# Kernel optimization log

Measured on AMD Instinct MI355X. Metric: run time of the kernel, lower is better.

The kernel has to match this reference:

```python
import jax, jax.numpy as jnp
import numpy as np

N = 100000
E = 1600000
D_IN = 256
N_HEADS = 4
OUT_SZ = 32  # output_dim // n_heads = 128 // 4
ALPHA = 0.2  # leaky relu slope


def setup_inputs() -> dict:
    key = jax.random.key(0)
    ks = jax.random.split(key, 8)
    x = jax.random.normal(ks[0], (N, D_IN), dtype=jnp.float32)
    edge_row = jax.random.randint(ks[1], (E,), 0, N, dtype=jnp.int32)
    edge_col = jax.random.randint(ks[2], (E,), 0, N, dtype=jnp.int32)
    # per-head params: W (conv1d k=1, no bias), a1/a2 (conv1d k=1 with bias)
    W = jax.random.normal(ks[3], (N_HEADS, D_IN, OUT_SZ), dtype=jnp.float32) * (1.0 / np.sqrt(D_IN))
    a1 = jax.random.normal(ks[4], (N_HEADS, OUT_SZ), dtype=jnp.float32) * (1.0 / np.sqrt(OUT_SZ))
    b1 = jnp.zeros((N_HEADS,), dtype=jnp.float32)
    a2 = jax.random.normal(ks[5], (N_HEADS, OUT_SZ), dtype=jnp.float32) * (1.0 / np.sqrt(OUT_SZ))
    b2 = jnp.zeros((N_HEADS,), dtype=jnp.float32)
    return {"x": x, "W": W, "a1": a1, "b1": b1, "a2": a2, "b2": b2,
            "edge_row": edge_row, "edge_col": edge_col}


def _gat_heads(x, W, a1, b1, a2, b2, edge_row, edge_col):
    # per-head linear transform: [H, N, O]
    fts = jnp.einsum('nd,hdo->hno', x, W)
    f1 = jnp.einsum('hno,ho->hn', fts, a1) + b1[:, None]  # [H, N]
    f2 = jnp.einsum('hno,ho->hn', fts, a2) + b2[:, None]  # [H, N]
    # edge logits: f1[row] + f2[col]  (adj values are 1)
    logits = f1[:, edge_row] + f2[:, edge_col]            # [H, E]
    lr = jnp.maximum(ALPHA * logits, logits)
    # segment softmax over each node's incoming edge set (rows)
    seg_max = jax.vmap(lambda v: jax.ops.segment_max(v, edge_row, num_segments=N))(lr)
    ex = jnp.exp(lr - seg_max[:, edge_row])
    denom = jax.vmap(lambda v: jax.ops.segment_sum(v, edge_row, num_segments=N))(ex)
    coef = ex / denom[:, edge_row]                        # [H, E]
    # SpMM aggregation: out[h, i] = sum_{e: row(e)=i} coef[h,e] * fts[h, col(e)]
    msg = coef[:, :, None] * fts[:, edge_col, :]          # [H, E, O]
    agg = jax.vmap(lambda m: jax.ops.segment_sum(m, edge_row, num_segments=N))(msg)  # [H, N, O]
    h = jnp.transpose(agg, (1, 0, 2)).reshape(N, N_HEADS * OUT_SZ)  # concat heads
    return jax.nn.elu(h)[None]  # [1, N, output_dim]


def reference(x, W, a1, b1, a2, b2, edge_row, edge_col):
    return _gat_heads(x, W, a1, b1, a2, b2, edge_row, edge_col)
```

## Files before the change

### kernel.cpp

```cpp
#include <hip/hip_runtime.h>
#include <hip/hip_bf16.h>
#include <math.h>

#define ALPHA 0.2f
#define PB_EDGES 4096

typedef __attribute__((ext_vector_type(8))) short short8;
typedef __attribute__((ext_vector_type(4))) float floatx4;

__device__ __forceinline__ ushort f2bf(float f) {
    uint u = __float_as_uint(f);
    u += 0x7fff + ((u >> 16) & 1);
    return (ushort)(u >> 16);
}

__device__ __forceinline__ short8 pack8(float4 lo, float4 hi) {
    short8 r;
    r[0] = (short)f2bf(lo.x); r[1] = (short)f2bf(lo.y);
    r[2] = (short)f2bf(lo.z); r[3] = (short)f2bf(lo.w);
    r[4] = (short)f2bf(hi.x); r[5] = (short)f2bf(hi.y);
    r[6] = (short)f2bf(hi.z); r[7] = (short)f2bf(hi.w);
    return r;
}

__global__ __launch_bounds__(256) void k_wprep(const float* __restrict__ W,
                                               ushort* __restrict__ Wt)
{
    int g = blockIdx.x * 256 + threadIdx.x;
    int c = g >> 8, d = g & 255;
    Wt[g] = f2bf(W[(c >> 5) * 8192 + d * 32 + (c & 31)]);
}

__global__ __launch_bounds__(256) void k_gemm(const float* __restrict__ x,
                                              const ushort* __restrict__ Wt,
                                              const float* __restrict__ a1v,
                                              const float* __restrict__ b1v,
                                              const float* __restrict__ a2v,
                                              const float* __restrict__ b2v,
                                              ushort* __restrict__ fts2,
                                              float* __restrict__ f1,
                                              float* __restrict__ f2, int M)
{
    __shared__ __align__(16) ushort smem[32768];
    const int t  = threadIdx.x;
    const int m0 = blockIdx.x * 128;

#pragma unroll
    for (int i = 0; i < 16; i++) {
        int f = i * 256 + t;
        int lane_ = f & 63, ksct = f >> 6;
        int ks = ksct & 7, ct = ksct >> 3;
        int mm = lane_ & 15, qq = lane_ >> 4;
        *(uint4*)&smem[f * 8] = *(const uint4*)&Wt[(ct * 16 + mm) * 256 + ks * 32 + qq * 8];
    }

    const int w = t >> 6, lane = t & 63;
    const int mm = lane & 15, qq = lane >> 4;

    int row0 = m0 + w * 32 + mm;
    int row1 = row0 + 16;
    int r0c = (row0 < M) ? row0 : (M - 1);
    int r1c = (row1 < M) ? row1 : (M - 1);
    const float* ar0 = x + (size_t)r0c * 256 + qq * 8;
    const float* ar1 = x + (size_t)r1c * 256 + qq * 8;
    short8 afrag[2][8];
#pragma unroll
    for (int ks = 0; ks < 8; ks++) {
        float4 lo0 = *(const float4*)(ar0 + ks * 32);
        float4 hi0 = *(const float4*)(ar0 + ks * 32 + 4);
        float4 lo1 = *(const float4*)(ar1 + ks * 32);
        float4 hi1 = *(const float4*)(ar1 + ks * 32 + 4);
        afrag[0][ks] = pack8(lo0, hi0);
        afrag[1][ks] = pack8(lo1, hi1);
    }

    floatx4 acc[2][8];
#pragma unroll
    for (int r = 0; r < 2; r++)
#pragma unroll
        for (int ct = 0; ct < 8; ct++) acc[r][ct] = (floatx4){0.f, 0.f, 0.f, 0.f};

    __syncthreads();

#pragma unroll
    for (int ks = 0; ks < 8; ks++) {
#pragma unroll
        for (int ct = 0; ct < 8; ct++) {
            short8 b8 = *(const short8*)&smem[((ct * 8 + ks) * 64 + lane) * 8];
            acc[0][ct] = __builtin_amdgcn_mfma_f32_16x16x32_bf16(afrag[0][ks], b8, acc[0][ct], 0, 0, 0);
            acc[1][ct] = __builtin_amdgcn_mfma_f32_16x16x32_bf16(afrag[1][ks], b8, acc[1][ct], 0, 0, 0);
        }
    }

    __syncthreads();
    ushort* ftsL = smem;
#pragma unroll
    for (int r = 0; r < 2; r++)
#pragma unroll
        for (int ct = 0; ct < 8; ct++)
#pragma unroll
            for (int i = 0; i < 4; i++) {
                int rowl = w * 32 + r * 16 + qq * 4 + i;
                ftsL[rowl * 136 + ct * 16 + mm] = f2bf(acc[r][ct][i]);
            }
    __syncthreads();

    {
        int rowl = t >> 1, half = t & 1;
        int gr = m0 + rowl;
        if (gr < M) {
            const uint4* src = (const uint4*)&ftsL[rowl * 136 + half * 64];
            uint4* dst = (uint4*)(fts2 + (size_t)gr * 128 + half * 64);
#pragma unroll
            for (int i = 0; i < 8; i++) dst[i] = src[i];
        }
    }
#pragma unroll
    for (int p = 0; p < 2; p++) {
        int task = p * 256 + t;
        int rowl = task >> 2, h = task & 3;
        int gr = m0 + rowl;
        if (gr < M) {
            const ushort* fr = &ftsL[rowl * 136 + h * 32];
            float s1 = 0.f, s2 = 0.f;
#pragma unroll
            for (int o = 0; o < 32; o++) {
                float v = __uint_as_float((uint)fr[o] << 16);
                s1 = fmaf(v, a1v[h * 32 + o], s1);
                s2 = fmaf(v, a2v[h * 32 + o], s2);
            }
            f1[gr * 4 + h] = s1 + b1v[h];
            f2[gr * 4 + h] = s2 + b2v[h];
        }
    }
}

__global__ __launch_bounds__(256) void k_phist(const int* __restrict__ erow,
                                               int* __restrict__ bcnt, int E, int NB)
{
    __shared__ int h[512];
    for (int i = threadIdx.x; i < 512; i += 256) h[i] = 0;
    __syncthreads();
    int b0 = blockIdx.x * PB_EDGES;
    int bend = b0 + PB_EDGES; if (bend > E) bend = E;
    for (int j = b0 + threadIdx.x; j < bend; j += 256)
        atomicAdd(&h[erow[j] >> 8], 1);
    __syncthreads();
    for (int i = threadIdx.x; i < NB; i += 256)
        if (h[i]) atomicAdd(&bcnt[i], h[i]);
}

__global__ __launch_bounds__(256) void k_scan_buckets(const int* __restrict__ bcnt,
                                                      int* __restrict__ base,
                                                      int* __restrict__ bcursor,
                                                      int NB, int E)
{
    __shared__ int s[256];
    int t = threadIdx.x;
    int i0 = 2 * t, i1 = 2 * t + 1;
    int v0 = (i0 < NB) ? bcnt[i0] : 0;
    int v1 = (i1 < NB) ? bcnt[i1] : 0;
    int tsum = v0 + v1;
    s[t] = tsum;
    __syncthreads();
    for (int off = 1; off < 256; off <<= 1) {
        int u = (t >= off) ? s[t - off] : 0;
        __syncthreads();
        s[t] += u;
        __syncthreads();
    }
    int excl = s[t] - tsum;
    if (i0 < NB) { base[i0] = excl;      bcursor[i0] = excl; }
    if (i1 < NB) { base[i1] = excl + v0; bcursor[i1] = excl + v0; }
    if (t == 0) base[NB] = E;
}

__global__ __launch_bounds__(256) void k_pscatter(const int* __restrict__ erow,
                                                  const int* __restrict__ ecol,
                                                  int* __restrict__ bcursor,
                                                  uint* __restrict__ part, int E)
{
    __shared__ int h[512];
    __shared__ int cur[512];
    for (int i = threadIdx.x; i < 512; i += 256) h[i] = 0;
    __syncthreads();
    int b0 = blockIdx.x * PB_EDGES;
    int bend = b0 + PB_EDGES; if (bend > E) bend = E;
    for (int j = b0 + threadIdx.x; j < bend; j += 256)
        atomicAdd(&h[erow[j] >> 8], 1);
    __syncthreads();
    for (int i = threadIdx.x; i < 512; i += 256)
        cur[i] = h[i] ? atomicAdd(&bcursor[i], h[i]) : 0;
    __syncthreads();
    for (int j = b0 + threadIdx.x; j < bend; j += 256) {
        int r = erow[j], c = ecol[j];
        int p = atomicAdd(&cur[r >> 8], 1);
        part[p] = ((uint)(r & 255) << 24) | (uint)c;
    }
}

__global__ __launch_bounds__(256) void k_bucket(const uint* __restrict__ part,
                                                const int* __restrict__ base,
                                                int* __restrict__ row_start,
                                                int* __restrict__ col_sorted,
                                                int Nn, int NB, int E)
{
    __shared__ int cnt[256];
    __shared__ int s[256];
    __shared__ int cur[256];
    const int b = blockIdx.x, t = threadIdx.x;
    const int start = base[b], end = base[b + 1];

    cnt[t] = 0;
    __syncthreads();
    for (int j = start + t; j < end; j += 256)
        atomicAdd(&cnt[part[j] >> 24], 1);
    __syncthreads();
    int v = cnt[t];
    s[t] = v;
    __syncthreads();
    for (int off = 1; off < 256; off <<= 1) {
        int u = (t >= off) ? s[t - off] : 0;
        __syncthreads();
        s[t] += u;
        __syncthreads();
    }
    int excl = s[t] - v;
    int r = b * 256 + t;
    if (r < Nn) row_start[r] = start + excl;
    if (b == 0 && t == 0) row_start[Nn] = E;
    cur[t] = start + excl;
    __syncthreads();
    for (int j = start + t; j < end; j += 256) {
        uint rc = part[j];
        int p = atomicAdd(&cur[rc >> 24], 1);
        col_sorted[p] = (int)(rc & 0xffffffu);
    }
}

__global__ __launch_bounds__(256) void k_gat_row(const ushort* __restrict__ fts2,
                                                 const float4* __restrict__ f1,
                                                 const float4* __restrict__ f2,
                                                 const int* __restrict__ row_start,
                                                 const int* __restrict__ cols,
                                                 float* __restrict__ out, int Nn)
{
    __shared__ __align__(16) float eL[4][256];
    __shared__ uint vL[4][64];

    const int wid  = threadIdx.x >> 6;
    const int lane = threadIdx.x & 63;
    const int r = blockIdx.x * 4 + wid;
    if (r >= Nn) return;

    const int s = row_start[r], e = row_start[r + 1];

    const int slot = lane >> 4;
    const int sub  = lane & 15;
    const int hsel = sub >> 2;

    float4* dst = (float4*)(out + (size_t)r * 128 + sub * 8);
    if (s == e) {
        if (slot == 0) {
            dst[0] = make_float4(0.f, 0.f, 0.f, 0.f);
            dst[1] = make_float4(0.f, 0.f, 0.f, 0.f);
        }
        return;
    }

    const float4 f1r = f1[r];
    float ds0 = 0.f, ds1 = 0.f, ds2 = 0.f, ds3 = 0.f;
    float acc[8];
#pragma unroll
    for (int i = 0; i < 8; i++) acc[i] = 0.f;

    const float* eBase   = &eL[wid][slot * 4 + hsel];
    const uint*  vBase   = &vL[wid][slot];
    const char*  ftsB    = (const char*)fts2;
    const uint   laneOff = (uint)sub * 16;

    for (int j0 = s; j0 < e; j0 += 64) {
        int j = j0 + lane;
        bool act = (j < e);
        int c = act ? cols[j] : 0;
        float4 f2v = f2[c];
        float l0 = f1r.x + f2v.x; l0 = fmaxf(l0, ALPHA * l0);
        float l1 = f1r.y + f2v.y; l1 = fmaxf(l1, ALPHA * l1);
        float l2 = f1r.z + f2v.z; l2 = fmaxf(l2, ALPHA * l2);
        float l3 = f1r.w + f2v.w; l3 = fmaxf(l3, ALPHA * l3);
        float e0 = act ? __expf(l0) : 0.f;
        float e1 = act ? __expf(l1) : 0.f;
        float e2 = act ? __expf(l2) : 0.f;
        float e3 = act ? __expf(l3) : 0.f;
        ds0 += e0; ds1 += e1; ds2 += e2; ds3 += e3;

        asm volatile("s_waitcnt lgkmcnt(0)" ::: "memory");
        ((float4*)eL[wid])[lane] = make_float4(e0, e1, e2, e3);
        vL[wid][lane] = (uint)c << 8;
        asm volatile("s_waitcnt lgkmcnt(0)" ::: "memory");

        int len = e - j0; if (len > 64) len = 64;
        int ng = (len + 3) >> 2;
#pragma unroll 4
        for (int g = 0; g < ng; g++) {
            float ee = eBase[g * 16];
            uint  vo = vBase[g * 4] + laneOff;
            uint4 vv = *(const uint4*)(ftsB + vo);
            float ve;
            ve = __uint_as_float(vv.x << 16);          acc[0] = fmaf(ee, ve, acc[0]);
            ve = __uint_as_float(vv.x & 0xffff0000u);  acc[1] = fmaf(ee, ve, acc[1]);
            ve = __uint_as_float(vv.y << 16);          acc[2] = fmaf(ee, ve, acc[2]);
            ve = __uint_as_float(vv.y & 0xffff0000u);  acc[3] = fmaf(ee, ve, acc[3]);
            ve = __uint_as_float(vv.z << 16);          acc[4] = fmaf(ee, ve, acc[4]);
            ve = __uint_as_float(vv.z & 0xffff0000u);  acc[5] = fmaf(ee, ve, acc[5]);
            ve = __uint_as_float(vv.w << 16);          acc[6] = fmaf(ee, ve, acc[6]);
            ve = __uint_as_float(vv.w & 0xffff0000u);  acc[7] = fmaf(ee, ve, acc[7]);
        }
    }

#pragma unroll
    for (int i = 0; i < 8; i++) {
        acc[i] += __shfl_xor(acc[i], 16, 64);
        acc[i] += __shfl_xor(acc[i], 32, 64);
    }
#pragma unroll
    for (int off = 32; off > 0; off >>= 1) {
        ds0 += __shfl_xor(ds0, off, 64);
        ds1 += __shfl_xor(ds1, off, 64);
        ds2 += __shfl_xor(ds2, off, 64);
        ds3 += __shfl_xor(ds3, off, 64);
    }
    float dsel = (hsel == 0) ? ds0 : (hsel == 1) ? ds1 : (hsel == 2) ? ds2 : ds3;
    float rinv = 1.0f / dsel;

    float o[8];
#pragma unroll
    for (int i = 0; i < 8; i++) {
        float v = acc[i] * rinv;
        o[i] = (v > 0.f) ? v : (__expf(v) - 1.0f);
    }
    if (slot == 0) {
        dst[0] = make_float4(o[0], o[1], o[2], o[3]);
        dst[1] = make_float4(o[4], o[5], o[6], o[7]);
    }
}

extern "C" void kernel_launch(void* const* d_in, const int* in_sizes, int n_in,
                              void* d_out, int out_size, void* d_ws, size_t ws_size,
                              hipStream_t stream)
{
    const float* x   = (const float*)d_in[0];
    const float* W   = (const float*)d_in[1];
    const float* a1  = (const float*)d_in[2];
    const float* b1  = (const float*)d_in[3];
    const float* a2  = (const float*)d_in[4];
    const float* b2  = (const float*)d_in[5];
    const int*   erow = (const int*)d_in[6];
    const int*   ecol = (const int*)d_in[7];
    float* out = (float*)d_out;

    const int N = in_sizes[0] / 256;
    const int E = in_sizes[6];
    const int NB = (N + 255) >> 8;

    char*  ws  = (char*)d_ws;
    size_t off = 0;
    auto carve = [&](size_t bytes) -> char* {
        char* p = ws + off;
        off += (bytes + 255) & ~(size_t)255;
        return p;
    };
    ushort* fts2      = (ushort*)carve((size_t)N * 128 * 2);
    ushort* Wt        = (ushort*)carve((size_t)128 * 256 * 2);
    float*  f1        = (float*)carve((size_t)N * 4 * 4);
    float*  f2        = (float*)carve((size_t)N * 4 * 4);
    int*    row_start = (int*)carve(((size_t)N + 1) * 4);
    int*    bcnt      = (int*)carve(512 * 4);
    int*    base      = (int*)carve(513 * 4);
    int*    bcursor   = (int*)carve(512 * 4);
    int*    col_sorted= (int*)carve((size_t)E * 4);
    uint*   part      = (uint*)carve((size_t)E * 4);
    (void)ws_size;

    k_wprep<<<128, 256, 0, stream>>>(W, Wt);
    k_gemm<<<(N + 127) / 128, 256, 0, stream>>>(x, Wt, a1, b1, a2, b2, fts2, f1, f2, N);

    hipMemsetAsync(bcnt, 0, 512 * 4, stream);
    int npb = (E + PB_EDGES - 1) / PB_EDGES;
    k_phist<<<npb, 256, 0, stream>>>(erow, bcnt, E, NB);
    k_scan_buckets<<<1, 256, 0, stream>>>(bcnt, base, bcursor, NB, E);
    k_pscatter<<<npb, 256, 0, stream>>>(erow, ecol, bcursor, part, E);
    k_bucket<<<NB, 256, 0, stream>>>(part, base, row_start, col_sorted, N, NB, E);

    k_gat_row<<<(N + 3) / 4, 256, 0, stream>>>(fts2, (const float4*)f1, (const float4*)f2,
                                               row_start, col_sorted, out, N);
}
```

Before: 341.9 us.

## Process four rows per wavefront in GAT row aggregation kernel

Remaps the row-aggregation kernel so each 64-lane wave handles four consecutive rows, one 16-lane slot per row. Edge attention weights are computed cooperatively over the joint edge range and staged in larger shared buffers. Each slot then accumulates its own row's messages and denominator directly. This removes the cross-slot shuffle reductions and the idle lanes that came from low-degree rows. In exchange, each slot runs a longer serial loop, and load balance can suffer when degrees within a group differ.

```diff
diff --git a/kernel.cpp b/kernel.cpp
--- a/kernel.cpp
+++ b/kernel.cpp
@@ -4,6 +4,7 @@
 
 #define ALPHA 0.2f
 #define PB_EDGES 4096
+#define MAXT 256
 
 typedef __attribute__((ext_vector_type(8))) short short8;
 typedef __attribute__((ext_vector_type(4))) float floatx4;
@@ -245,67 +246,78 @@
                                                  const int* __restrict__ cols,
                                                  float* __restrict__ out, int Nn)
 {
-    __shared__ __align__(16) float eL[4][256];
-    __shared__ uint vL[4][64];
+    __shared__ __align__(16) float eLs[4][MAXT * 4];
+    __shared__ uint vLs[4][MAXT];
 
     const int wid  = threadIdx.x >> 6;
     const int lane = threadIdx.x & 63;
-    const int r = blockIdx.x * 4 + wid;
-    if (r >= Nn) return;
-
-    const int s = row_start[r], e = row_start[r + 1];
-
     const int slot = lane >> 4;
     const int sub  = lane & 15;
     const int hsel = sub >> 2;
 
-    float4* dst = (float4*)(out + (size_t)r * 128 + sub * 8);
-    if (s == e) {
-        if (slot == 0) {
-            dst[0] = make_float4(0.f, 0.f, 0.f, 0.f);
-            dst[1] = make_float4(0.f, 0.f, 0.f, 0.f);
-        }
-        return;
-    }
-
-    const float4 f1r = f1[r];
-    float ds0 = 0.f, ds1 = 0.f, ds2 = 0.f, ds3 = 0.f;
+    const int rbase = (blockIdx.x * 4 + wid) * 4;
+    if (rbase >= Nn) return;
+
+    const int myr = rbase + slot;
+    const bool rowAct = (myr < Nn);
+    const int i0 = rowAct ? myr : Nn;
+    const int i1 = (myr + 1 < Nn) ? (myr + 1) : Nn;
+    const int sB = row_start[i0];
+    const int eB = row_start[i1];
+    const int degTot = eB - sB;
+
+    const int s0 = __shfl(sB, 0, 64);
+    const int b1 = __shfl(sB, 16, 64);
+    const int b2 = __shfl(sB, 32, 64);
+    const int b3 = __shfl(sB, 48, 64);
+    const int T  = __shfl(eB, 48, 64) - s0;
+
+    float ds = 0.f;
     float acc[8];
 #pragma unroll
     for (int i = 0; i < 8; i++) acc[i] = 0.f;
 
-    const float* eBase   = &eL[wid][slot * 4 + hsel];
-    const uint*  vBase   = &vL[wid][slot];
-    const char*  ftsB    = (const char*)fts2;
-    const uint   laneOff = (uint)sub * 16;
-
-    for (int j0 = s; j0 < e; j0 += 64) {
-        int j = j0 + lane;
-        bool act = (j < e);
-        int c = act ? cols[j] : 0;
-        float4 f2v = f2[c];
-        float l0 = f1r.x + f2v.x; l0 = fmaxf(l0, ALPHA * l0);
-        float l1 = f1r.y + f2v.y; l1 = fmaxf(l1, ALPHA * l1);
-        float l2 = f1r.z + f2v.z; l2 = fmaxf(l2, ALPHA * l2);
-        float l3 = f1r.w + f2v.w; l3 = fmaxf(l3, ALPHA * l3);
-        float e0 = act ? __expf(l0) : 0.f;
-        float e1 = act ? __expf(l1) : 0.f;
-        float e2 = act ? __expf(l2) : 0.f;
-        float e3 = act ? __expf(l3) : 0.f;
-        ds0 += e0; ds1 += e1; ds2 += e2; ds3 += e3;
-
+    const char* ftsB = (const char*)fts2;
+    const uint  laneOff = (uint)sub * 16;
+    float* eLw = eLs[wid];
+    uint*  vLw = vLs[wid];
+
+    for (int base = 0; base < T; base += MAXT) {
+        int tc = T - base; if (tc > MAXT) tc = MAXT;
+        int tcPad = (tc + 63) & ~63;
+
+        for (int lt = lane; lt < tcPad; lt += 64) {
+            bool act = (lt < tc);
+            int j = s0 + base + lt;
+            int c = act ? cols[j] : 0;
+            int rsel = (j >= b1) + (j >= b2) + (j >= b3);
+            int fi = rbase + rsel; if (fi >= Nn) fi = Nn - 1;
+            float4 f1r = f1[fi];
+            float4 f2v = f2[c];
+            float l0 = f1r.x + f2v.x; l0 = fmaxf(l0, ALPHA * l0);
+            float l1 = f1r.y + f2v.y; l1 = fmaxf(l1, ALPHA * l1);
+            float l2 = f1r.z + f2v.z; l2 = fmaxf(l2, ALPHA * l2);
+            float l3 = f1r.w + f2v.w; l3 = fmaxf(l3, ALPHA * l3);
+            float e0 = act ? __expf(l0) : 0.f;
+            float e1 = act ? __expf(l1) : 0.f;
+            float e2 = act ? __expf(l2) : 0.f;
+            float e3 = act ? __expf(l3) : 0.f;
+            asm volatile("s_waitcnt lgkmcnt(0)" ::: "memory");
+            *(float4*)&eLw[lt * 4] = make_float4(e0, e1, e2, e3);
+            vLw[lt] = (uint)c << 8;
+        }
         asm volatile("s_waitcnt lgkmcnt(0)" ::: "memory");
-        ((float4*)eL[wid])[lane] = make_float4(e0, e1, e2, e3);
-        vL[wid][lane] = (uint)c << 8;
-        asm volatile("s_waitcnt lgkmcnt(0)" ::: "memory");
-
-        int len = e - j0; if (len > 64) len = 64;
-        int ng = (len + 3) >> 2;
+
+        int lo = sB - s0 - base; lo = (lo < 0) ? 0 : ((lo > tc) ? tc : lo);
+        int hi = eB - s0 - base; hi = (hi < 0) ? 0 : ((hi > tc) ? tc : hi);
+        int ni = hi - lo;
+        int eIdx = lo * 4 + hsel;
 #pragma unroll 4
-        for (int g = 0; g < ng; g++) {
-            float ee = eBase[g * 16];
-            uint  vo = vBase[g * 4] + laneOff;
+        for (int g = 0; g < ni; g++) {
+            float ee = eLw[eIdx + g * 4];
+            uint  vo = vLw[lo + g] + laneOff;
             uint4 vv = *(const uint4*)(ftsB + vo);
+            ds += ee;
             float ve;
             ve = __uint_as_float(vv.x << 16);          acc[0] = fmaf(ee, ve, acc[0]);
             ve = __uint_as_float(vv.x & 0xffff0000u);  acc[1] = fmaf(ee, ve, acc[1]);
@@ -318,28 +330,16 @@
         }
     }
 
-#pragma unroll
-    for (int i = 0; i < 8; i++) {
-        acc[i] += __shfl_xor(acc[i], 16, 64);
-        acc[i] += __shfl_xor(acc[i], 32, 64);
-    }
-#pragma unroll
-    for (int off = 32; off > 0; off >>= 1) {
-        ds0 += __shfl_xor(ds0, off, 64);
-        ds1 += __shfl_xor(ds1, off, 64);
-        ds2 += __shfl_xor(ds2, off, 64);
-        ds3 += __shfl_xor(ds3, off, 64);
-    }
-    float dsel = (hsel == 0) ? ds0 : (hsel == 1) ? ds1 : (hsel == 2) ? ds2 : ds3;
+    float dsel = (degTot > 0) ? ds : 1.f;
     float rinv = 1.0f / dsel;
-
     float o[8];
 #pragma unroll
     for (int i = 0; i < 8; i++) {
         float v = acc[i] * rinv;
         o[i] = (v > 0.f) ? v : (__expf(v) - 1.0f);
     }
-    if (slot == 0) {
+    if (rowAct) {
+        float4* dst = (float4*)(out + (size_t)myr * 128 + sub * 8);
         dst[0] = make_float4(o[0], o[1], o[2], o[3]);
         dst[1] = make_float4(o[4], o[5], o[6], o[7]);
     }
@@ -392,6 +392,6 @@
     k_pscatter<<<npb, 256, 0, stream>>>(erow, ecol, bcursor, part, E);
     k_bucket<<<NB, 256, 0, stream>>>(part, base, row_start, col_sorted, N, NB, E);
 
-    k_gat_row<<<(N + 3) / 4, 256, 0, stream>>>(fts2, (const float4*)f1, (const float4*)f2,
-                                               row_start, col_sorted, out, N);
-}
+    k_gat_row<<<(N + 15) / 16, 256, 0, stream>>>(fts2, (const float4*)f1, (const float4*)f2,
+                                                 row_start, col_sorted, out, N);
+}
```

New measurement: 337.3 us. No clear change (-1.4%).
